# Performance work log

Hardware: AMD Instinct MI355X
Metric: run time of the kernel (lower is better)

The kernel has to match this reference:

```python
import jax, jax.numpy as jnp
import numpy as np

H, HKV, D, HID = 32, 8, 128, 4096
EPS = 1e-6
ROPE_BASE = 10000.0
SCALE = D ** -0.5


def setup_inputs() -> dict:
    key = jax.random.key(0)
    ks = jax.random.split(key, 4)
    T = 2048
    x = jax.random.normal(ks[0], (T, HID), dtype=jnp.float32)
    w_qkv = jax.random.normal(ks[1], ((H + 2 * HKV) * D, HID), dtype=jnp.float32) * (HID ** -0.5)
    b_qkv = jax.random.normal(ks[2], ((H + 2 * HKV) * D,), dtype=jnp.float32) * 0.02
    q_norm_w = jnp.ones((D,), dtype=jnp.float32)
    k_norm_w = jnp.ones((D,), dtype=jnp.float32)
    w_o = jax.random.normal(ks[3], (HID, H * D), dtype=jnp.float32) * ((H * D) ** -0.5)
    return {"x": x, "w_qkv": w_qkv, "b_qkv": b_qkv, "q_norm_w": q_norm_w,
            "k_norm_w": k_norm_w, "w_o": w_o}


def _rms_norm(t, w):
    # per-head RMSNorm over the last (head_dim) axis
    var = jnp.mean(t * t, axis=-1, keepdims=True)
    return t * jax.lax.rsqrt(var + EPS) * w


def _rope(t, cos, sin):
    # neox-style half rotation; cos/sin: [T, D//2], t: [T, h, D]
    t1, t2 = jnp.split(t, 2, axis=-1)
    c = cos[:, None, :]
    s = sin[:, None, :]
    return jnp.concatenate([t1 * c - t2 * s, t2 * c + t1 * s], axis=-1)


def reference(x, w_qkv, b_qkv, q_norm_w, k_norm_w, w_o):
    T = x.shape[0]
    qkv = x @ w_qkv.T + b_qkv                      # [T, (H+2*HKV)*D]
    q, k, v = jnp.split(qkv, [H * D, (H + HKV) * D], axis=-1)
    q = q.reshape(T, H, D)
    k = k.reshape(T, HKV, D)
    v = v.reshape(T, HKV, D)

    # QK RMSNorm
    q = _rms_norm(q, q_norm_w)
    k = _rms_norm(k, k_norm_w)

    # rotary embedding, base 10000, full head_dim
    pos = jnp.arange(T, dtype=jnp.float32)
    inv_freq = 1.0 / (ROPE_BASE ** (jnp.arange(0, D, 2, dtype=jnp.float32) / D))
    freqs = pos[:, None] * inv_freq[None, :]        # [T, D//2]
    cos, sin = jnp.cos(freqs), jnp.sin(freqs)
    q = _rope(q, cos, sin)
    k = _rope(k, cos, sin)

    # GQA: kv_head_mapping = arange(HKV).repeat_interleave(H // HKV)
    groups = H // HKV
    k = jnp.repeat(k, groups, axis=1)               # [T, H, D]
    v = jnp.repeat(v, groups, axis=1)

    scores = jnp.einsum('thd,shd->hts', q, k) * SCALE   # [H, T, T]
    causal = jnp.tril(jnp.ones((T, T), dtype=bool))
    scores = jnp.where(causal[None], scores, jnp.finfo(scores.dtype).min)
    probs = jax.nn.softmax(scores, axis=-1)
    out = jnp.einsum('hts,shd->thd', probs, v)      # [T, H, D]
    return out.reshape(T, H * D) @ w_o.T            # [T, HID]
```

## Files before the change

kernel.cpp:

```cpp
#include <hip/hip_runtime.h>
#include <stdint.h>
#include <stddef.h>

typedef __bf16 bf16_t;
typedef __bf16 bf16x8 __attribute__((ext_vector_type(8)));
typedef float  f32x4  __attribute__((ext_vector_type(4)));

#define T_SEQ 2048
#define NH    32
#define NKV   8
#define DH    128
#define HIDN  4096
#define NQKV  6144
#define SCALE 0.08838834764831845f
#define C1_EXP2 0.12751743187767f
#define C2_EXP2 16.590992970223f

__device__ inline float b2f(bf16_t v) {
  uint32_t u = ((uint32_t)__builtin_bit_cast(uint16_t, v)) << 16;
  return __builtin_bit_cast(float, u);
}
__device__ inline bf16_t f2b(float f) { return (bf16_t)f; }
__device__ inline void gl_lds16(const void* g, void* l) {
  __builtin_amdgcn_global_load_lds(
      (__attribute__((address_space(1))) void*)g,
      (__attribute__((address_space(3))) void*)l, 16, 0, 0);
}
__device__ inline f32x4 mfma16(bf16x8 a, bf16x8 b, f32x4 c) {
  return __builtin_amdgcn_mfma_f32_16x16x32_bf16(a, b, c, 0, 0, 0);
}
__device__ inline void store_val(float* p, float v)  { *p = v; }
__device__ inline void store_val(bf16_t* p, float v) { *p = f2b(v); }

__global__ __launch_bounds__(256)
void cvt2_kernel(const float* __restrict__ a, bf16_t* __restrict__ ao, int na,
                 const float* __restrict__ b, bf16_t* __restrict__ bo) {
  int blk = blockIdx.x;
  const float* in;
  bf16_t* out;
  int rb;
  if (blk < na) { in = a; out = ao; rb = blk; }
  else          { in = b; out = bo; rb = blk - na; }
  size_t i = ((size_t)rb * 256 + threadIdx.x) * 8;
  f32x4 va = *(const f32x4*)(in + i);
  f32x4 vb = *(const f32x4*)(in + i + 4);
  bf16x8 o;
#pragma unroll
  for (int e = 0; e < 4; ++e) { o[e] = f2b(va[e]); o[e + 4] = f2b(vb[e]); }
  *(bf16x8*)(out + i) = o;
}

template <bool BIAS, typename TOUT>
__global__ __launch_bounds__(256)
void gemm_bt(const bf16_t* __restrict__ A, const bf16_t* __restrict__ Bw,
             const float* __restrict__ bias, TOUT* __restrict__ C,
             int M, int N, int K) {
  __shared__ __align__(16) char smem[32768];
  char* sA = smem;
  char* sB = smem + 16384;
  const int tid  = threadIdx.x;
  const int lane = tid & 63, wave = tid >> 6;
  const int quad = lane >> 4, l16 = lane & 15;
  const int wm = wave >> 1, wn = wave & 1;
  const int m0 = blockIdx.y * 128, n0 = blockIdx.x * 128;

  f32x4 acc[4][4] = {};
  const int kTiles = K >> 6;

  for (int kt = 0; kt < kTiles; ++kt) {
    const int kb = kt << 6;
#pragma unroll
    for (int i = 0; i < 4; ++i) {
      int p = i * 256 + tid;
      int row = p >> 3, gc = (p & 7) ^ (row & 7);
      gl_lds16(A  + (size_t)(m0 + row) * K + kb + gc * 8, sA + p * 16);
      gl_lds16(Bw + (size_t)(n0 + row) * K + kb + gc * 8, sB + p * 16);
    }
    __syncthreads();

#pragma unroll
    for (int ks = 0; ks < 2; ++ks) {
      bf16x8 af[4], bfr[4];
      const int c = ks * 4 + quad;
#pragma unroll
      for (int i = 0; i < 4; ++i) {
        int ra = wm * 64 + i * 16 + l16;
        af[i]  = *(const bf16x8*)(sA + ra * 128 + ((c ^ (ra & 7)) * 16));
        int rb = wn * 64 + i * 16 + l16;
        bfr[i] = *(const bf16x8*)(sB + rb * 128 + ((c ^ (rb & 7)) * 16));
      }
#pragma unroll
      for (int i = 0; i < 4; ++i)
#pragma unroll
        for (int j = 0; j < 4; ++j)
          acc[i][j] = mfma16(af[i], bfr[j], acc[i][j]);
    }
    __syncthreads();
  }
#pragma unroll
  for (int i = 0; i < 4; ++i) {
    int mrow = m0 + wm * 64 + i * 16 + quad * 4;
#pragma unroll
    for (int j = 0; j < 4; ++j) {
      int ncol = n0 + wn * 64 + j * 16 + l16;
      float bv = BIAS ? bias[ncol] : 0.f;
#pragma unroll
      for (int r = 0; r < 4; ++r)
        store_val(&C[(size_t)(mrow + r) * N + ncol], acc[i][j][r] + bv);
    }
  }
}

#define PP_PREP_BLOCKS 20480
#define PP_VT_BLOCKS   512
#define PP_CVT_BLOCKS  8192
__global__ __launch_bounds__(256)
void postproc_kernel(const bf16_t* __restrict__ qkv,
                     const float* __restrict__ qw, const float* __restrict__ kw,
                     const float* __restrict__ wo,
                     bf16_t* __restrict__ Qp, bf16_t* __restrict__ Kp,
                     bf16_t* __restrict__ Vt, bf16_t* __restrict__ wob) {
  __shared__ bf16_t tile[64 * 66];
  const int bid = blockIdx.x;
  const int tid = threadIdx.x;

  if (bid < PP_PREP_BLOCKS) {
    const int id   = bid * 4 + (tid >> 6);
    const int lane = tid & 63;
    const int t = id / 40, slot = id % 40;
    const bf16_t* src = qkv + (size_t)t * NQKV + slot * DH;
    float x1 = b2f(src[lane]), x2 = b2f(src[lane + 64]);
    float ssq = x1 * x1 + x2 * x2;
#pragma unroll
    for (int m = 1; m < 64; m <<= 1) ssq += __shfl_xor(ssq, m, 64);
    float rms = rsqrtf(ssq * (1.f / 128.f) + 1e-6f);
    const float* w = (slot < 32) ? qw : kw;
    float n1 = x1 * rms * w[lane];
    float n2 = x2 * rms * w[lane + 64];
    float inv = exp2f(-0.20762050593046014f * (float)lane);
    float ang = (float)t * inv;
    float cs = __cosf(ang), sn = __sinf(ang);
    bf16_t* dst = (slot < 32) ? Qp + ((size_t)t * NH  + slot)        * DH
                              : Kp + ((size_t)t * NKV + (slot - 32)) * DH;
    dst[lane]      = f2b(n1 * cs - n2 * sn);
    dst[lane + 64] = f2b(n2 * cs + n1 * sn);
  } else if (bid < PP_PREP_BLOCKS + PP_VT_BLOCKS) {
    const int b = bid - PP_PREP_BLOCKS;
    const int t0 = (b & 31) * 64, d0 = ((b >> 5) & 1) * 64, kvh = b >> 6;
#pragma unroll
    for (int i = 0; i < 2; ++i) {
      int id = i * 256 + tid;
      int tr = id >> 3, dc = id & 7;
      bf16x8 v = *(const bf16x8*)(qkv + (size_t)(t0 + tr) * NQKV +
                                  (40 + kvh) * DH + d0 + dc * 8);
#pragma unroll
      for (int e = 0; e < 8; ++e) tile[tr * 66 + dc * 8 + e] = v[e];
    }
    __syncthreads();
#pragma unroll
    for (int i = 0; i < 2; ++i) {
      int id = i * 256 + tid;
      int dr = id >> 3, tc = id & 7;
      bf16x8 o;
#pragma unroll
      for (int e = 0; e < 8; ++e) o[e] = tile[(tc * 8 + e) * 66 + dr];
      *(bf16x8*)(Vt + ((size_t)kvh * DH + d0 + dr) * T_SEQ + t0 + tc * 8) = o;
    }
  } else {
    const int c = bid - (PP_PREP_BLOCKS + PP_VT_BLOCKS);
    size_t i = ((size_t)c * 256 + tid) * 8;
    f32x4 a = *(const f32x4*)(wo + i);
    f32x4 bq = *(const f32x4*)(wo + i + 4);
    bf16x8 o;
#pragma unroll
    for (int e = 0; e < 4; ++e) { o[e] = f2b(a[e]); o[e + 4] = f2b(bq[e]); }
    *(bf16x8*)(wob + i) = o;
  }
}

__global__ __launch_bounds__(256)
void attn_kernel(const bf16_t* __restrict__ Qp, const bf16_t* __restrict__ Kp,
                 const bf16_t* __restrict__ Vt, bf16_t* __restrict__ Out) {
  __shared__ __align__(16) char smem[73728];
  const int tid  = threadIdx.x;
  const int lane = tid & 63, wave = tid >> 6;
  const int quad = lane >> 4, l16 = lane & 15;
  const int b = blockIdx.x, h = blockIdx.y;
  const int qt_lo = b, qt_hi = 31 - b;
  const int kvh = h >> 2;
  char* sPw = smem + 65536 + wave * 2048;

  bf16x8 qf_lo[4], qf_hi[4];
  {
    const int row_lo = qt_lo * 64 + wave * 16 + l16;
    const int row_hi = qt_hi * 64 + wave * 16 + l16;
#pragma unroll
    for (int ks = 0; ks < 4; ++ks) {
      qf_lo[ks] = *(const bf16x8*)(Qp + ((size_t)row_lo * NH + h) * DH + ks * 32 + quad * 8);
      qf_hi[ks] = *(const bf16x8*)(Qp + ((size_t)row_hi * NH + h) * DH + ks * 32 + quad * 8);
    }
  }
  f32x4 acc_lo[8] = {}, acc_hi[8] = {};
  float l_lo[4] = {0.f, 0.f, 0.f, 0.f}, l_hi[4] = {0.f, 0.f, 0.f, 0.f};

  auto stage = [&](int kt) {
    char* sK = smem + (kt & 1) * 16384;
    char* sV = smem + 32768 + (kt & 1) * 16384;
    const int k0 = kt * 64;
#pragma unroll
    for (int i = 0; i < 4; ++i) {
      int p = i * 256 + tid;
      int row = p >> 4, gc = (p & 15) ^ (row & 15);
      gl_lds16(Kp + ((size_t)(k0 + row) * NKV + kvh) * DH + gc * 8, sK + p * 16);
    }
#pragma unroll
    for (int i = 0; i < 4; ++i) {
      int p = i * 256 + tid;
      int d = p >> 3, gc = (p & 7) ^ (d & 7);
      gl_lds16(Vt + ((size_t)kvh * DH + d) * T_SEQ + k0 + gc * 8, sV + p * 16);
    }
  };

  auto compute = [&](const bf16x8 (&qf)[4], f32x4 (&acc)[8], float (&lrow)[4],
                     int qt, int kt, char* sK, char* sVT) {
    f32x4 sfr[4] = {};
#pragma unroll
    for (int ks = 0; ks < 4; ++ks) {
      const int c = ks * 4 + quad;
#pragma unroll
      for (int j = 0; j < 4; ++j) {
        int row = j * 16 + l16;
        bf16x8 kf = *(const bf16x8*)(sK + row * 256 + ((c ^ (row & 15)) * 16));
        sfr[j] = mfma16(qf[ks], kf, sfr[j]);
      }
    }
    float sv[4][4];
    const bool diag = (kt == qt);
#pragma unroll
    for (int j = 0; j < 4; ++j)
#pragma unroll
      for (int r = 0; r < 4; ++r) {
        float e = exp2f(fmaf(sfr[j][r], C1_EXP2, -C2_EXP2));
        if (diag) {
          int qg = wave * 16 + quad * 4 + r;
          int kg = j * 16 + l16;
          if (kg > qg) e = 0.f;
        }
        sv[j][r] = e;
      }
#pragma unroll
    for (int r = 0; r < 4; ++r)
      lrow[r] += (sv[0][r] + sv[1][r]) + (sv[2][r] + sv[3][r]);
#pragma unroll
    for (int j = 0; j < 4; ++j)
#pragma unroll
      for (int r = 0; r < 4; ++r) {
        int prow = quad * 4 + r;
        int col  = j * 16 + l16;
        int c    = col >> 3;
        ((bf16_t*)(sPw + prow * 128 + ((c ^ (prow & 7)) * 16)))[col & 7] = f2b(sv[j][r]);
      }
    __asm__ volatile("" ::: "memory");
    bf16x8 pf[2];
#pragma unroll
    for (int ks2 = 0; ks2 < 2; ++ks2) {
      int c = ks2 * 4 + quad;
      pf[ks2] = *(const bf16x8*)(sPw + l16 * 128 + ((c ^ (l16 & 7)) * 16));
    }
    __asm__ volatile("" ::: "memory");
#pragma unroll
    for (int j2 = 0; j2 < 8; ++j2)
#pragma unroll
      for (int ks2 = 0; ks2 < 2; ++ks2) {
        int d = j2 * 16 + l16;
        int c = ks2 * 4 + quad;
        bf16x8 vf = *(const bf16x8*)(sVT + d * 128 + ((c ^ (d & 7)) * 16));
        acc[j2] = mfma16(pf[ks2], vf, acc[j2]);
      }
  };

  stage(0);
  for (int kt = 0; kt <= qt_hi; ++kt) {
    __syncthreads();
    if (kt < qt_hi) stage(kt + 1);
    char* sK  = smem + (kt & 1) * 16384;
    char* sVT = smem + 32768 + (kt & 1) * 16384;
    compute(qf_hi, acc_hi, l_hi, qt_hi, kt, sK, sVT);
    if (kt <= qt_lo)
      compute(qf_lo, acc_lo, l_lo, qt_lo, kt, sK, sVT);
  }

#pragma unroll
  for (int r = 0; r < 4; ++r) {
    float lh = l_hi[r], ll = l_lo[r];
#pragma unroll
    for (int m = 1; m < 16; m <<= 1) {
      lh += __shfl_xor(lh, m, 64);
      ll += __shfl_xor(ll, m, 64);
    }
    float inv_h = 1.f / lh, inv_l = 1.f / ll;
    int qg_h = qt_hi * 64 + wave * 16 + quad * 4 + r;
    int qg_l = qt_lo * 64 + wave * 16 + quad * 4 + r;
#pragma unroll
    for (int j2 = 0; j2 < 8; ++j2) {
      int d = j2 * 16 + l16;
      Out[(size_t)qg_h * (NH * DH) + h * DH + d] = f2b(acc_hi[j2][r] * inv_h);
      Out[(size_t)qg_l * (NH * DH) + h * DH + d] = f2b(acc_lo[j2][r] * inv_l);
    }
  }
}

extern "C" void kernel_launch(void* const* d_in, const int* in_sizes, int n_in,
                              void* d_out, int out_size, void* d_ws, size_t ws_size,
                              hipStream_t stream) {
  const float* x    = (const float*)d_in[0];
  const float* wqkv = (const float*)d_in[1];
  const float* bqkv = (const float*)d_in[2];
  const float* qnw  = (const float*)d_in[3];
  const float* knw  = (const float*)d_in[4];
  const float* wo   = (const float*)d_in[5];
  float* out = (float*)d_out;

  char* ws = (char*)d_ws;
  bf16_t* wqkvb = (bf16_t*)(ws);
  bf16_t* xb    = (bf16_t*)(ws + 50331648);
  bf16_t* qkv   = (bf16_t*)(ws + 67108864);
  bf16_t* Qp    = (bf16_t*)(ws);
  bf16_t* Kp    = (bf16_t*)(ws + 16777216);
  bf16_t* Vt    = (bf16_t*)(ws + 20971520);
  bf16_t* wob   = (bf16_t*)(ws + 25165824);
  bf16_t* At    = (bf16_t*)(ws + 67108864);

  cvt2_kernel<<<16384, 256, 0, stream>>>(x, xb, 4096, wqkv, wqkvb);
  gemm_bt<true, bf16_t><<<dim3(NQKV / 128, T_SEQ / 128), 256, 0, stream>>>(
      xb, wqkvb, bqkv, qkv, T_SEQ, NQKV, HIDN);
  postproc_kernel<<<PP_PREP_BLOCKS + PP_VT_BLOCKS + PP_CVT_BLOCKS, 256, 0, stream>>>(
      qkv, qnw, knw, wo, Qp, Kp, Vt, wob);
  attn_kernel<<<dim3(16, NH), 256, 0, stream>>>(Qp, Kp, Vt, At);
  gemm_bt<false, float><<<dim3(HIDN / 128, T_SEQ / 128), 256, 0, stream>>>(
      At, wob, nullptr, out, T_SEQ, HIDN, HIDN);
}
```

Measured before the change: 553.8 us.

## Split attention blocks per query tile and read V fragments directly from global

The attention kernel no longer pairs a low and a high query tile per block. It launches one block per query tile (32x32 grid, largest tiles first), shrinking LDS usage and raising occupancy. V is no longer staged into LDS: each lane loads its transposed-V fragments straight from global memory, relying on cache reuse across waves and blocks of the same KV head. This trades the balanced pairing and the LDS staging of V for more blocks and lower LDS pressure, and it risks uneven block lengths and exposed global-load latency in the PV MFMA loop.

```diff
diff --git a/kernel.cpp b/kernel.cpp
--- a/kernel.cpp
+++ b/kernel.cpp
@@ -181,31 +181,27 @@
 __global__ __launch_bounds__(256)
 void attn_kernel(const bf16_t* __restrict__ Qp, const bf16_t* __restrict__ Kp,
                  const bf16_t* __restrict__ Vt, bf16_t* __restrict__ Out) {
-  __shared__ __align__(16) char smem[73728];
+  __shared__ __align__(16) char smem[40960];
   const int tid  = threadIdx.x;
   const int lane = tid & 63, wave = tid >> 6;
   const int quad = lane >> 4, l16 = lane & 15;
-  const int b = blockIdx.x, h = blockIdx.y;
-  const int qt_lo = b, qt_hi = 31 - b;
+  const int qt = 31 - blockIdx.x, h = blockIdx.y;
   const int kvh = h >> 2;
-  char* sPw = smem + 65536 + wave * 2048;
-
-  bf16x8 qf_lo[4], qf_hi[4];
+  char* sPw = smem + 32768 + wave * 2048;
+  const bf16_t* Vbase = Vt + (size_t)kvh * DH * T_SEQ;
+
+  bf16x8 qf[4];
   {
-    const int row_lo = qt_lo * 64 + wave * 16 + l16;
-    const int row_hi = qt_hi * 64 + wave * 16 + l16;
-#pragma unroll
-    for (int ks = 0; ks < 4; ++ks) {
-      qf_lo[ks] = *(const bf16x8*)(Qp + ((size_t)row_lo * NH + h) * DH + ks * 32 + quad * 8);
-      qf_hi[ks] = *(const bf16x8*)(Qp + ((size_t)row_hi * NH + h) * DH + ks * 32 + quad * 8);
-    }
-  }
-  f32x4 acc_lo[8] = {}, acc_hi[8] = {};
-  float l_lo[4] = {0.f, 0.f, 0.f, 0.f}, l_hi[4] = {0.f, 0.f, 0.f, 0.f};
+    const int row = qt * 64 + wave * 16 + l16;
+#pragma unroll
+    for (int ks = 0; ks < 4; ++ks)
+      qf[ks] = *(const bf16x8*)(Qp + ((size_t)row * NH + h) * DH + ks * 32 + quad * 8);
+  }
+  f32x4 acc[8] = {};
+  float lrow[4] = {0.f, 0.f, 0.f, 0.f};
 
   auto stage = [&](int kt) {
     char* sK = smem + (kt & 1) * 16384;
-    char* sV = smem + 32768 + (kt & 1) * 16384;
     const int k0 = kt * 64;
 #pragma unroll
     for (int i = 0; i < 4; ++i) {
@@ -213,16 +209,15 @@
       int row = p >> 4, gc = (p & 15) ^ (row & 15);
       gl_lds16(Kp + ((size_t)(k0 + row) * NKV + kvh) * DH + gc * 8, sK + p * 16);
     }
-#pragma unroll
-    for (int i = 0; i < 4; ++i) {
-      int p = i * 256 + tid;
-      int d = p >> 3, gc = (p & 7) ^ (d & 7);
-      gl_lds16(Vt + ((size_t)kvh * DH + d) * T_SEQ + k0 + gc * 8, sV + p * 16);
-    }
   };
 
-  auto compute = [&](const bf16x8 (&qf)[4], f32x4 (&acc)[8], float (&lrow)[4],
-                     int qt, int kt, char* sK, char* sVT) {
+  stage(0);
+  for (int kt = 0; kt <= qt; ++kt) {
+    __syncthreads();
+    if (kt < qt) stage(kt + 1);
+    char* sK = smem + (kt & 1) * 16384;
+    const int k0 = kt * 64;
+
     f32x4 sfr[4] = {};
 #pragma unroll
     for (int ks = 0; ks < 4; ++ks) {
@@ -269,43 +264,29 @@
     }
     __asm__ volatile("" ::: "memory");
 #pragma unroll
-    for (int j2 = 0; j2 < 8; ++j2)
-#pragma unroll
-      for (int ks2 = 0; ks2 < 2; ++ks2) {
-        int d = j2 * 16 + l16;
-        int c = ks2 * 4 + quad;
-        bf16x8 vf = *(const bf16x8*)(sVT + d * 128 + ((c ^ (d & 7)) * 16));
-        acc[j2] = mfma16(pf[ks2], vf, acc[j2]);
-      }
-  };
-
-  stage(0);
-  for (int kt = 0; kt <= qt_hi; ++kt) {
-    __syncthreads();
-    if (kt < qt_hi) stage(kt + 1);
-    char* sK  = smem + (kt & 1) * 16384;
-    char* sVT = smem + 32768 + (kt & 1) * 16384;
-    compute(qf_hi, acc_hi, l_hi, qt_hi, kt, sK, sVT);
-    if (kt <= qt_lo)
-      compute(qf_lo, acc_lo, l_lo, qt_lo, kt, sK, sVT);
-  }
-
-#pragma unroll
-  for (int r = 0; r < 4; ++r) {
-    float lh = l_hi[r], ll = l_lo[r];
-#pragma unroll
-    for (int m = 1; m < 16; m <<= 1) {
-      lh += __shfl_xor(lh, m, 64);
-      ll += __shfl_xor(ll, m, 64);
-    }
-    float inv_h = 1.f / lh, inv_l = 1.f / ll;
-    int qg_h = qt_hi * 64 + wave * 16 + quad * 4 + r;
-    int qg_l = qt_lo * 64 + wave * 16 + quad * 4 + r;
-#pragma unroll
     for (int j2 = 0; j2 < 8; ++j2) {
       int d = j2 * 16 + l16;
-      Out[(size_t)qg_h * (NH * DH) + h * DH + d] = f2b(acc_hi[j2][r] * inv_h);
-      Out[(size_t)qg_l * (NH * DH) + h * DH + d] = f2b(acc_lo[j2][r] * inv_l);
+      const bf16_t* vrow = Vbase + (size_t)d * T_SEQ + k0;
+#pragma unroll
+      for (int ks2 = 0; ks2 < 2; ++ks2) {
+        int c = ks2 * 4 + quad;
+        bf16x8 vf = *(const bf16x8*)(vrow + c * 8);
+        acc[j2] = mfma16(pf[ks2], vf, acc[j2]);
+      }
+    }
+  }
+
+#pragma unroll
+  for (int r = 0; r < 4; ++r) {
+    float lv = lrow[r];
+#pragma unroll
+    for (int m = 1; m < 16; m <<= 1) lv += __shfl_xor(lv, m, 64);
+    float inv = 1.f / lv;
+    int qg = qt * 64 + wave * 16 + quad * 4 + r;
+#pragma unroll
+    for (int j2 = 0; j2 < 8; ++j2) {
+      int d = j2 * 16 + l16;
+      Out[(size_t)qg * (NH * DH) + h * DH + d] = f2b(acc[j2][r] * inv);
     }
   }
 }
@@ -336,7 +317,7 @@
       xb, wqkvb, bqkv, qkv, T_SEQ, NQKV, HIDN);
   postproc_kernel<<<PP_PREP_BLOCKS + PP_VT_BLOCKS + PP_CVT_BLOCKS, 256, 0, stream>>>(
       qkv, qnw, knw, wo, Qp, Kp, Vt, wob);
-  attn_kernel<<<dim3(16, NH), 256, 0, stream>>>(Qp, Kp, Vt, At);
+  attn_kernel<<<dim3(32, NH), 256, 0, stream>>>(Qp, Kp, Vt, At);
   gemm_bt<false, float><<<dim3(HIDN / 128, T_SEQ / 128), 256, 0, stream>>>(
       At, wob, nullptr, out, T_SEQ, HIDN, HIDN);
 }
```

Result: slower. 682.7 us (+23.3%).
